# Kernel tuning notes

Measured on AMD Instinct MI355X. Metric: run time of the kernel, lower is better.

Reference implementation:

```python
import jax, jax.numpy as jnp
import numpy as np

NUM_CLASSES = 88
DICE_W, CE_W = 0.6, 0.4
SMOOTH = 1e-5  # MONAI DiceLoss smooth_nr = smooth_dr = 1e-5


def setup_inputs() -> dict:
    key = jax.random.key(0)
    k1, k2 = jax.random.split(key)
    B, C, D, H, W = 2, NUM_CLASSES, 96, 96, 96
    pred = jax.random.normal(k1, (B, C, D, H, W), dtype=jnp.float32)
    target = jax.random.randint(k2, (B, D, H, W), 0, NUM_CLASSES, dtype=jnp.int32)
    return {"pred": pred, "target": target}


def reference(pred, target):
    # pred: [B, C, D, H, W] logits; target: [B, D, H, W] int labels, -1 = ignore
    valid = target != -1                                  # [B,D,H,W]
    tgt = jnp.where(valid, target, 0).astype(jnp.int32)

    # --- CrossEntropyLoss(ignore_index=-1), mean over valid voxels ---
    logp = jax.nn.log_softmax(pred, axis=1)               # [B,C,D,H,W]
    nll = -jnp.take_along_axis(logp, tgt[:, None], axis=1)[:, 0]  # [B,D,H,W]
    vf = valid.astype(pred.dtype)
    ce = jnp.sum(nll * vf) / jnp.maximum(jnp.sum(vf), 1.0)

    # --- one-hot target with ignore mask; mask applied to pred for dice ---
    one_hot = jax.nn.one_hot(tgt, NUM_CLASSES, axis=1, dtype=pred.dtype)
    one_hot = one_hot * vf[:, None]                       # [B,C,D,H,W]
    pred_m = pred * vf[:, None]

    # --- MONAI DiceLoss: softmax=True, squared_pred=True, include_background,
    #     reduce over spatial dims, mean over (batch, channel) ---
    probs = jax.nn.softmax(pred_m, axis=1)
    sp_axes = (2, 3, 4)
    inter = jnp.sum(one_hot * probs, axis=sp_axes)        # [B,C]
    ground_o = jnp.sum(one_hot * one_hot, axis=sp_axes)   # [B,C]
    pred_o = jnp.sum(probs * probs, axis=sp_axes)         # [B,C]
    dice = 1.0 - (2.0 * inter + SMOOTH) / (ground_o + pred_o + SMOOTH)
    dice = jnp.mean(dice)

    return CE_W * ce + DICE_W * dice
```

## Files before the change

### kernel.cpp

```cpp
#include <hip/hip_runtime.h>

#define NCLS 88
#define DHW (96 * 96 * 96)
#define TPB 256
#define CPW 22
#define VPJ 256
#define NJ 2
#define VOX_PER_BLOCK (VPJ * NJ)
#define BLOCKS_PER_B (DHW / VOX_PER_BLOCK)
#define SLOTS 32
#define SMOOTH 1e-5f
#define WS_PER_SLOT 529

typedef __fp16 h2 __attribute__((ext_vector_type(2)));
typedef float f2 __attribute__((ext_vector_type(2)));
union H2I { h2 h; int i; };

__device__ __forceinline__ float wave_reduce_sum(float v) {
#pragma unroll
    for (int i = 1; i < 64; i <<= 1)
        v += __shfl_xor(v, i, 64);
    return v;
}

__device__ __forceinline__ h2 wave_reduce_h2(h2 v) {
#pragma unroll
    for (int i = 1; i < 64; i <<= 1) {
        H2I u; u.h = v;
        u.i = __shfl_xor(u.i, i, 64);
        v = v + u.h;
    }
    return v;
}

__global__ __launch_bounds__(TPB)
void seg_loss_main(const float* __restrict__ pred, const int* __restrict__ tgt,
                   float* __restrict__ ws) {
    __shared__ float s_inter[NCLS];
    __shared__ float s_pred[NCLS];
    __shared__ float s_cnt[NCLS];
    __shared__ float s_ce;
    __shared__ float2 s_ex[NJ][4][4][64];

    const int tid  = threadIdx.x;
    const int lane = tid & 63;
    const int wave = tid >> 6;
    const int b    = blockIdx.x / BLOCKS_PER_B;
    const int base = (blockIdx.x % BLOCKS_PER_B) * VOX_PER_BLOCK;
    const int cls0 = wave * CPW;
    const float* pb = pred + (size_t)b * NCLS * DHW + (size_t)cls0 * DHW;
    const int*   tb = tgt  + (size_t)b * DHW;

    if (tid < NCLS) { s_inter[tid] = 0.f; s_pred[tid] = 0.f; s_cnt[tid] = 0.f; }
    if (tid == 0) s_ce = 0.f;
    __syncthreads();

    h2 acc[CPW / 2];
#pragma unroll
    for (int i = 0; i < CPW / 2; ++i) acc[i] = (h2){(__fp16)0.f, (__fp16)0.f};
    float ce_acc = 0.f;

    for (int j = 0; j < NJ; ++j) {
        const int vox = base + j * VPJ + lane * 4;
        const int4 t4 = *(const int4*)(tb + vox);
        const int tv[4] = { t4.x, t4.y, t4.z, t4.w };
        bool  val[4]; int tc[4]; float vf[4];
#pragma unroll
        for (int v = 0; v < 4; ++v) {
            val[v] = (tv[v] != -1);
            tc[v]  = val[v] ? tv[v] : 0;
            vf[v]  = val[v] ? 1.f : 0.f;
        }
        const float* p = pb + vox;

        float sA[4] = {0,0,0,0}, sB[4] = {0,0,0,0};
        float eta[4] = {0,0,0,0}, etb[4] = {0,0,0,0};
        int ef[CPW];
#pragma unroll
        for (int c = 0; c < CPW; ++c) {
            const float4 x = *(const float4*)(p + (size_t)c * DHW);
            const float e0 = __expf(x.x * vf[0]);
            const float e1 = __expf(x.y * vf[1]);
            const float e2 = __expf(x.z * vf[2]);
            const float e3 = __expf(x.w * vf[3]);
            const int cc = cls0 + c;
            if (c & 1) {
                sB[0] += e0; sB[1] += e1; sB[2] += e2; sB[3] += e3;
                etb[0] = (cc == tc[0]) ? e0 : etb[0];
                etb[1] = (cc == tc[1]) ? e1 : etb[1];
                etb[2] = (cc == tc[2]) ? e2 : etb[2];
                etb[3] = (cc == tc[3]) ? e3 : etb[3];
            } else {
                sA[0] += e0; sA[1] += e1; sA[2] += e2; sA[3] += e3;
                eta[0] = (cc == tc[0]) ? e0 : eta[0];
                eta[1] = (cc == tc[1]) ? e1 : eta[1];
                eta[2] = (cc == tc[2]) ? e2 : eta[2];
                eta[3] = (cc == tc[3]) ? e3 : eta[3];
            }
            const int lo = __builtin_amdgcn_cvt_pk_fp8_f32(e0, e1, 0, false);
            ef[c] = __builtin_amdgcn_cvt_pk_fp8_f32(e2, e3, lo, true);
        }

#pragma unroll
        for (int v = 0; v < 4; ++v)
            s_ex[j][wave][v][lane] = make_float2(sA[v] + sB[v], eta[v] + etb[v]);
        __syncthreads();

        float inv[4], pt[4];
#pragma unroll
        for (int v = 0; v < 4; ++v) {
            const float2 q0 = s_ex[j][0][v][lane];
            const float2 q1 = s_ex[j][1][v][lane];
            const float2 q2 = s_ex[j][2][v][lane];
            const float2 q3 = s_ex[j][3][v][lane];
            const float s1 = (q0.x + q1.x) + (q2.x + q3.x);
            const float et = (q0.y + q1.y) + (q2.y + q3.y);
            inv[v] = 1.f / s1;
            pt[v]  = et * inv[v];
        }

#pragma unroll
        for (int v = 0; v < 4; ++v) {
            const bool own = (tc[v] >= cls0) && (tc[v] < cls0 + CPW);
            if (val[v] && own) {
                ce_acc -= __logf(pt[v]);
                atomicAdd(&s_inter[tc[v]], pt[v]);
                atomicAdd(&s_cnt[tc[v]], 1.f);
            }
        }

#pragma unroll
        for (int q = 0; q < CPW / 2; ++q) {
            const f2 lo0 = __builtin_amdgcn_cvt_pk_f32_fp8(ef[2 * q],     false);
            const f2 hi0 = __builtin_amdgcn_cvt_pk_f32_fp8(ef[2 * q],     true);
            const f2 lo1 = __builtin_amdgcn_cvt_pk_f32_fp8(ef[2 * q + 1], false);
            const f2 hi1 = __builtin_amdgcn_cvt_pk_f32_fp8(ef[2 * q + 1], true);
            const float a0 = lo0.x * inv[0], a1 = lo0.y * inv[1];
            const float a2 = hi0.x * inv[2], a3 = hi0.y * inv[3];
            const float b0 = lo1.x * inv[0], b1 = lo1.y * inv[1];
            const float b2 = hi1.x * inv[2], b3 = hi1.y * inv[3];
            const float sq0 = (a0 * a0 + a1 * a1) + (a2 * a2 + a3 * a3);
            const float sq1 = (b0 * b0 + b1 * b1) + (b2 * b2 + b3 * b3);
            acc[q] += __builtin_amdgcn_cvt_pkrtz(sq0, sq1);
        }
    }

#pragma unroll
    for (int i = 0; i < CPW / 2; ++i) {
        h2 r = wave_reduce_h2(acc[i]);
        if (lane == 0) {
            s_pred[cls0 + 2 * i]     += (float)r.x;
            s_pred[cls0 + 2 * i + 1] += (float)r.y;
        }
    }
    ce_acc = wave_reduce_sum(ce_acc);
    if (lane == 0) atomicAdd(&s_ce, ce_acc);

    __syncthreads();

    float* wsl = ws + (size_t)(blockIdx.x & (SLOTS - 1)) * WS_PER_SLOT;
    if (tid < NCLS) {
        atomicAdd(&wsl[0 * 176 + b * NCLS + tid], s_inter[tid]);
        atomicAdd(&wsl[1 * 176 + b * NCLS + tid], s_pred[tid]);
        atomicAdd(&wsl[2 * 176 + b * NCLS + tid], s_cnt[tid]);
    }
    if (tid == 0) atomicAdd(&wsl[528], s_ce);
}

__global__ __launch_bounds__(TPB)
void seg_loss_final(const float* __restrict__ ws, float* __restrict__ out) {
    const int tid = threadIdx.x;
    float dice = 0.f, cnt = 0.f;
    if (tid < 2 * NCLS) {
        float I = 0.f, P = 0.f, G = 0.f;
        for (int s = 0; s < SLOTS; ++s) {
            const float* w = ws + (size_t)s * WS_PER_SLOT;
            I += w[tid]; P += w[176 + tid]; G += w[352 + tid];
        }
        dice = 1.f - (2.f * I + SMOOTH) / (G + P + SMOOTH);
        cnt  = G;
    }
    float ce_s = 0.f;
    if (tid < SLOTS) ce_s = ws[(size_t)tid * WS_PER_SLOT + 528];

    dice = wave_reduce_sum(dice);
    cnt  = wave_reduce_sum(cnt);
    ce_s = wave_reduce_sum(ce_s);

    __shared__ float sd[4], sc2[4], se[4];
    const int w = tid >> 6, l = tid & 63;
    if (l == 0) { sd[w] = dice; sc2[w] = cnt; se[w] = ce_s; }
    __syncthreads();
    if (tid == 0) {
        const float D  = sd[0] + sd[1] + sd[2] + sd[3];
        const float Cn = sc2[0] + sc2[1] + sc2[2] + sc2[3];
        const float CE = (se[0] + se[1] + se[2] + se[3]) / fmaxf(Cn, 1.0f);
        out[0] = 0.4f * CE + 0.6f * (D / 176.f);
    }
}

extern "C" void kernel_launch(void* const* d_in, const int* in_sizes, int n_in,
                              void* d_out, int out_size, void* d_ws, size_t ws_size,
                              hipStream_t stream) {
    const float* pred = (const float*)d_in[0];
    const int*   tgt  = (const int*)d_in[1];
    float* ws = (float*)d_ws;

    (void)hipMemsetAsync(d_ws, 0, SLOTS * WS_PER_SLOT * sizeof(float), stream);
    seg_loss_main<<<2 * BLOCKS_PER_B, TPB, 0, stream>>>(pred, tgt, ws);
    seg_loss_final<<<1, TPB, 0, stream>>>(ws, (float*)d_out);
}
```

Measured before the change: 140.6 us.

## Split classes across eight waves per block and use fp32 square-sum accumulators

Each block now runs 512 threads as eight waves, and each wave handles 11 classes instead of 22. The goal is fewer loads and fewer registers in flight per wave, which should give more memory-level parallelism and better occupancy on this bandwidth-bound pass. The packed fp16 accumulators for the squared-probability sums are replaced by per-class fp32 accumulators with plain float wave reductions. The cross-wave softmax reduction through shared memory now sums eight partials instead of four, which adds some LDS traffic per voxel.

```diff
diff --git a/kernel.cpp b/kernel.cpp
--- a/kernel.cpp
+++ b/kernel.cpp
@@ -2,8 +2,9 @@
 
 #define NCLS 88
 #define DHW (96 * 96 * 96)
-#define TPB 256
-#define CPW 22
+#define TPB 512
+#define WAVES 8
+#define CPW 11
 #define VPJ 256
 #define NJ 2
 #define VOX_PER_BLOCK (VPJ * NJ)
@@ -12,24 +13,12 @@
 #define SMOOTH 1e-5f
 #define WS_PER_SLOT 529
 
-typedef __fp16 h2 __attribute__((ext_vector_type(2)));
 typedef float f2 __attribute__((ext_vector_type(2)));
-union H2I { h2 h; int i; };
 
 __device__ __forceinline__ float wave_reduce_sum(float v) {
 #pragma unroll
     for (int i = 1; i < 64; i <<= 1)
         v += __shfl_xor(v, i, 64);
-    return v;
-}
-
-__device__ __forceinline__ h2 wave_reduce_h2(h2 v) {
-#pragma unroll
-    for (int i = 1; i < 64; i <<= 1) {
-        H2I u; u.h = v;
-        u.i = __shfl_xor(u.i, i, 64);
-        v = v + u.h;
-    }
     return v;
 }
 
@@ -40,7 +29,7 @@
     __shared__ float s_pred[NCLS];
     __shared__ float s_cnt[NCLS];
     __shared__ float s_ce;
-    __shared__ float2 s_ex[NJ][4][4][64];
+    __shared__ float2 s_ex[NJ][WAVES][4][64];
 
     const int tid  = threadIdx.x;
     const int lane = tid & 63;
@@ -55,9 +44,9 @@
     if (tid == 0) s_ce = 0.f;
     __syncthreads();
 
-    h2 acc[CPW / 2];
+    float acc[CPW];
 #pragma unroll
-    for (int i = 0; i < CPW / 2; ++i) acc[i] = (h2){(__fp16)0.f, (__fp16)0.f};
+    for (int i = 0; i < CPW; ++i) acc[i] = 0.f;
     float ce_acc = 0.f;
 
     for (int j = 0; j < NJ; ++j) {
@@ -109,12 +98,12 @@
         float inv[4], pt[4];
 #pragma unroll
         for (int v = 0; v < 4; ++v) {
-            const float2 q0 = s_ex[j][0][v][lane];
-            const float2 q1 = s_ex[j][1][v][lane];
-            const float2 q2 = s_ex[j][2][v][lane];
-            const float2 q3 = s_ex[j][3][v][lane];
-            const float s1 = (q0.x + q1.x) + (q2.x + q3.x);
-            const float et = (q0.y + q1.y) + (q2.y + q3.y);
+            float s1 = 0.f, et = 0.f;
+#pragma unroll
+            for (int w = 0; w < WAVES; ++w) {
+                const float2 q = s_ex[j][w][v][lane];
+                s1 += q.x; et += q.y;
+            }
             inv[v] = 1.f / s1;
             pt[v]  = et * inv[v];
         }
@@ -130,28 +119,19 @@
         }
 
 #pragma unroll
-        for (int q = 0; q < CPW / 2; ++q) {
-            const f2 lo0 = __builtin_amdgcn_cvt_pk_f32_fp8(ef[2 * q],     false);
-            const f2 hi0 = __builtin_amdgcn_cvt_pk_f32_fp8(ef[2 * q],     true);
-            const f2 lo1 = __builtin_amdgcn_cvt_pk_f32_fp8(ef[2 * q + 1], false);
-            const f2 hi1 = __builtin_amdgcn_cvt_pk_f32_fp8(ef[2 * q + 1], true);
-            const float a0 = lo0.x * inv[0], a1 = lo0.y * inv[1];
-            const float a2 = hi0.x * inv[2], a3 = hi0.y * inv[3];
-            const float b0 = lo1.x * inv[0], b1 = lo1.y * inv[1];
-            const float b2 = hi1.x * inv[2], b3 = hi1.y * inv[3];
-            const float sq0 = (a0 * a0 + a1 * a1) + (a2 * a2 + a3 * a3);
-            const float sq1 = (b0 * b0 + b1 * b1) + (b2 * b2 + b3 * b3);
-            acc[q] += __builtin_amdgcn_cvt_pkrtz(sq0, sq1);
+        for (int c = 0; c < CPW; ++c) {
+            const f2 lo = __builtin_amdgcn_cvt_pk_f32_fp8(ef[c], false);
+            const f2 hi = __builtin_amdgcn_cvt_pk_f32_fp8(ef[c], true);
+            const float a0 = lo.x * inv[0], a1 = lo.y * inv[1];
+            const float a2 = hi.x * inv[2], a3 = hi.y * inv[3];
+            acc[c] += (a0 * a0 + a1 * a1) + (a2 * a2 + a3 * a3);
         }
     }
 
 #pragma unroll
-    for (int i = 0; i < CPW / 2; ++i) {
-        h2 r = wave_reduce_h2(acc[i]);
-        if (lane == 0) {
-            s_pred[cls0 + 2 * i]     += (float)r.x;
-            s_pred[cls0 + 2 * i + 1] += (float)r.y;
-        }
+    for (int c = 0; c < CPW; ++c) {
+        const float r = wave_reduce_sum(acc[c]);
+        if (lane == 0) s_pred[cls0 + c] += r;
     }
     ce_acc = wave_reduce_sum(ce_acc);
     if (lane == 0) atomicAdd(&s_ce, ce_acc);
@@ -167,7 +147,7 @@
     if (tid == 0) atomicAdd(&wsl[528], s_ce);
 }
 
-__global__ __launch_bounds__(TPB)
+__global__ __launch_bounds__(256)
 void seg_loss_final(const float* __restrict__ ws, float* __restrict__ out) {
     const int tid = threadIdx.x;
     float dice = 0.f, cnt = 0.f;
@@ -208,5 +188,5 @@
 
     (void)hipMemsetAsync(d_ws, 0, SLOTS * WS_PER_SLOT * sizeof(float), stream);
     seg_loss_main<<<2 * BLOCKS_PER_B, TPB, 0, stream>>>(pred, tgt, ws);
-    seg_loss_final<<<1, TPB, 0, stream>>>(ws, (float*)d_out);
+    seg_loss_final<<<1, 256, 0, stream>>>(ws, (float*)d_out);
 }
```

Result: slower. 186.9 us (+33.0%).
